# Optimization experiments

Measured on AMD Instinct MI355X. Metric: run time of the kernel, lower is better.

Reference implementation:

```python
import jax, jax.numpy as jnp
import numpy as np

K = 3  # sparsify_graph default k


def _lstm_dir(x, Wi, Wh, b, reverse):
    # x: [B, T, Hin]; Wi: [Hin, 4H]; Wh: [H, 4H]; b: [4H]
    B = x.shape[0]
    H = Wh.shape[0]
    xs = jnp.swapaxes(x, 0, 1)  # [T, B, Hin]
    if reverse:
        xs = xs[::-1]

    def step(carry, xt):
        h, c = carry
        g = xt @ Wi + h @ Wh + b
        i, f, gg, o = jnp.split(g, 4, axis=-1)  # torch gate order i,f,g,o
        c = jax.nn.sigmoid(f) * c + jax.nn.sigmoid(i) * jnp.tanh(gg)
        h = jax.nn.sigmoid(o) * jnp.tanh(c)
        return (h, c), h

    h0 = jnp.zeros((B, H), x.dtype)
    _, hs = jax.lax.scan(step, (h0, h0), xs)
    if reverse:
        hs = hs[::-1]
    return jnp.swapaxes(hs, 0, 1)  # [B, T, H]


def setup_inputs() -> dict:
    key = jax.random.key(0)
    ks = jax.random.split(key, 24)
    B, T, C, F = 16, 256, 64, 128
    GO, H = 32, 32  # gat_out, lstm hidden
    s = 0.1
    return {
        "x": jax.random.normal(ks[0], (B, T, C, F), jnp.float32),
        "spectral_w": jax.random.normal(ks[1], (C, F), jnp.float32),
        "gat_W": jax.random.normal(ks[2], (F, GO), jnp.float32) * s,
        "gat_a": jax.random.normal(ks[3], (2 * GO,), jnp.float32),
        "pool_w": jax.random.normal(ks[4], (GO, 1), jnp.float32) * s,
        "pool_b": jnp.zeros((1,), jnp.float32),
        "lstm_Wi_f": jax.random.normal(ks[5], (GO, 4 * H), jnp.float32) * s,
        "lstm_Wh_f": jax.random.normal(ks[6], (H, 4 * H), jnp.float32) * s,
        "lstm_b_f": jnp.zeros((4 * H,), jnp.float32),
        "lstm_Wi_r": jax.random.normal(ks[7], (GO, 4 * H), jnp.float32) * s,
        "lstm_Wh_r": jax.random.normal(ks[8], (H, 4 * H), jnp.float32) * s,
        "lstm_b_r": jnp.zeros((4 * H,), jnp.float32),
        "ta_W": jax.random.normal(ks[9], (2 * H, 2 * H), jnp.float32) * s,
        "ta_b": jnp.zeros((2 * H,), jnp.float32),
        "ta_v": jax.random.normal(ks[10], (2 * H,), jnp.float32) * s,
        "ln_g": jnp.ones((2 * H,), jnp.float32),
        "ln_b": jnp.zeros((2 * H,), jnp.float32),
        "fc1_w": jax.random.normal(ks[11], (2 * H, 32), jnp.float32) * s,
        "fc1_b": jnp.zeros((32,), jnp.float32),
        "fc2_w": jax.random.normal(ks[12], (32, 3), jnp.float32) * s,
        "fc2_b": jnp.zeros((3,), jnp.float32),
    }


def reference(x, spectral_w, gat_W, gat_a, pool_w, pool_b,
              lstm_Wi_f, lstm_Wh_f, lstm_b_f, lstm_Wi_r, lstm_Wh_r, lstm_b_r,
              ta_W, ta_b, ta_v, ln_g, ln_b, fc1_w, fc1_b, fc2_w, fc2_b):
    B, T, C, F = x.shape
    # SpectralWeighting: per-(channel,feature) softmaxed weights over feature dim
    x = x * jax.nn.softmax(spectral_w, axis=-1)  # [B,T,C,F]

    # compute_graph per sample: mean_t of cosine-similarity Gram over channels
    Hn = x / (jnp.linalg.norm(x, axis=-1, keepdims=True) + 1e-8)
    A = jnp.einsum('btcf,btdf->bcd', Hn, Hn) / T  # [B,C,C]

    # sparsify_graph: per-row top-(K+1), drop diagonal, symmetrize mask
    _, idx = jax.lax.top_k(A, K + 1)  # [B,C,K+1]
    topk_mask = jnp.sum(jax.nn.one_hot(idx, C, dtype=jnp.float32), axis=2) > 0  # [B,C,C]
    eye = jnp.eye(C, dtype=bool)
    topk_mask = topk_mask & ~eye
    topk_mask = topk_mask | jnp.swapaxes(topk_mask, 1, 2)
    A = jnp.where(topk_mask, A, 0.0)

    # GAT layer, vectorized over (B, T) with shared per-sample adjacency
    Wh = jnp.einsum('btcf,fo->btco', x, gat_W)  # [B,T,C,32]
    O = Wh.shape[-1]
    s1 = Wh @ gat_a[:O]  # [B,T,C]  a . Wh_i
    s2 = Wh @ gat_a[O:]  # [B,T,C]  a . Wh_j
    e = jax.nn.leaky_relu(s1[..., :, None] + s2[..., None, :], 0.2)  # [B,T,C,C]
    amask = (A > 0) | eye  # [B,C,C]
    e = jnp.where(amask[:, None], e, -1e9)
    alpha = jax.nn.softmax(e, axis=-1)  # dropout skipped (eval mode)
    gat = jax.nn.relu(jnp.einsum('btcd,btdo->btco', alpha, Wh))  # [B,T,C,32]

    # ChannelAttentionPooling: softmax over channel dim
    w = jax.nn.softmax(gat @ pool_w + pool_b, axis=2)  # [B,T,C,1]
    h = jnp.sum(gat * w, axis=2)  # [B,T,32]

    # BiLSTM
    hf = _lstm_dir(h, lstm_Wi_f, lstm_Wh_f, lstm_b_f, False)
    hr = _lstm_dir(h, lstm_Wi_r, lstm_Wh_r, lstm_b_r, True)
    h = jnp.concatenate([hf, hr], axis=-1)  # [B,T,64]

    # TemporalAttention (dropout skipped, eval mode)
    sc = (jnp.tanh(h @ ta_W + ta_b) @ ta_v) / 1.5  # [B,T]
    al = jax.nn.softmax(sc, axis=1)
    ctx = jnp.sum(h * al[..., None], axis=1)  # [B,64]

    # LayerNorm
    mu = jnp.mean(ctx, axis=-1, keepdims=True)
    var = jnp.var(ctx, axis=-1, keepdims=True)
    ctx = (ctx - mu) / jnp.sqrt(var + 1e-5) * ln_g + ln_b

    # Classifier head (dropout skipped, eval mode)
    return jax.nn.relu(ctx @ fc1_w + fc1_b) @ fc2_w + fc2_b  # [B,3]
```

## Files before the change

### kernel.cpp

```cpp
#include <hip/hip_runtime.h>
#include <hip/hip_bf16.h>

#define B_  16
#define T_  256
#define C_  64
#define F_  128
#define O_  32
#define H_  32
#define G4_ 128

typedef __attribute__((ext_vector_type(8))) short bfrag;
typedef __attribute__((ext_vector_type(4))) float f4acc;
typedef __attribute__((ext_vector_type(2))) float f2;

__device__ __forceinline__ unsigned short f2bf(float v) {
    union { float f; unsigned u; } c; c.f = v;
    unsigned r = c.u + 0x7FFF + ((c.u >> 16) & 1);
    return (unsigned short)(r >> 16);
}
__device__ __forceinline__ float bf2f(unsigned short b) {
    union { float f; unsigned u; } c; c.u = ((unsigned)b) << 16; return c.f;
}
__device__ __forceinline__ float sigm_f(float x) {
    return __builtin_amdgcn_rcpf(1.f + __expf(-x));
}
__device__ __forceinline__ float tanh_f(float x) {
    float e = __expf(2.f * x);
    return 1.f - 2.f * __builtin_amdgcn_rcpf(e + 1.f);
}
__device__ __forceinline__ float readlane_f(float v, int l) {
    return __int_as_float(__builtin_amdgcn_readlane(__float_as_int(v), l));
}

__global__ __launch_bounds__(64) void k_sw(const float* __restrict__ w,
                                           float* __restrict__ sw) {
    int c = blockIdx.x, lane = threadIdx.x;
    const float* row = w + c * F_;
    float v0 = row[lane], v1 = row[lane + 64];
    float m = fmaxf(v0, v1);
#pragma unroll
    for (int s = 1; s < 64; s <<= 1) m = fmaxf(m, __shfl_xor(m, s));
    float e0 = __expf(v0 - m), e1 = __expf(v1 - m);
    float s = e0 + e1;
#pragma unroll
    for (int s_ = 1; s_ < 64; s_ <<= 1) s += __shfl_xor(s, s_);
    sw[c * F_ + lane] = e0 / s;
    sw[c * F_ + lane + 64] = e1 / s;
}

#define TCP 4
#define PSTR 136

#define MFMA16(a, b, c) __builtin_amdgcn_mfma_f32_16x16x32_bf16(a, b, c, 0, 0, 0)

__global__ __launch_bounds__(256) void k_phase1(
    const float* __restrict__ x, const float* __restrict__ sw,
    const float* __restrict__ gat_W, const float* __restrict__ gat_a,
    float* __restrict__ A, float* __restrict__ Wh,
    float* __restrict__ s1, float* __restrict__ s2) {
    const int b = blockIdx.x, tc = blockIdx.y, tid = threadIdx.x;
    const int wv = tid >> 6, lane = tid & 63;
    const int quad = lane >> 4, l16 = lane & 15;

    __shared__ unsigned short hhi[64 * PSTR];
    __shared__ unsigned short hlo[64 * PSTR];
    __shared__ float nrm[64];
    __shared__ float s1p[2][64], s2p[2][64];

    float4 swr[8];
    {
        const float4* sw4 = (const float4*)sw;
#pragma unroll
        for (int i = 0; i < 8; i++) swr[i] = sw4[tid + 256 * i];
    }

    const int rt0 = (wv >> 1) * 2;
    const int ct0 = (wv & 1) * 2;
    const int jW = wv & 1;

    bfrag wfh[4], wfl[4];
    {
        const int n = l16 + 16 * jW;
#pragma unroll
        for (int k = 0; k < 4; k++) {
            union { unsigned short u[8]; bfrag v; } Hu, Lu;
#pragma unroll
            for (int u = 0; u < 8; u++) {
                float v = gat_W[(32 * k + quad * 8 + u) * O_ + n];
                unsigned short hb = f2bf(v);
                Hu.u[u] = hb;
                Lu.u[u] = f2bf(v - bf2f(hb));
            }
            wfh[k] = Hu.v;
            wfl[k] = Lu.v;
        }
    }
    const float ga1 = gat_a[l16 + 16 * jW];
    const float ga2 = gat_a[O_ + l16 + 16 * jW];

    f4acc accA[2][2];
#pragma unroll
    for (int i = 0; i < 2; i++)
#pragma unroll
        for (int j = 0; j < 2; j++) accA[i][j] = (f4acc){0.f, 0.f, 0.f, 0.f};

    for (int tt = 0; tt < TCP; ++tt) {
        const int t = tc * TCP + tt;
        const float4* xg = (const float4*)(x + ((size_t)(b * T_ + t) << 13));
        float4 xr[8];
#pragma unroll
        for (int i = 0; i < 8; i++) xr[i] = xg[tid + 256 * i];

        __syncthreads();

        float invn_[8];
#pragma unroll
        for (int i = 0; i < 8; i++) {
            float4 v = xr[i], s = swr[i];
            v.x *= s.x; v.y *= s.y; v.z *= s.z; v.w *= s.w;
            xr[i] = v;
            float ss = v.x * v.x + v.y * v.y + v.z * v.z + v.w * v.w;
#pragma unroll
            for (int d = 1; d < 32; d <<= 1) ss += __shfl_xor(ss, d);
            float nv = sqrtf(ss) + 1e-8f;
            invn_[i] = 1.0f / nv;
            if ((tid & 31) == 0) nrm[(tid >> 5) + 8 * i] = nv;
        }
#pragma unroll
        for (int i = 0; i < 8; i++) {
            int c = (tid >> 5) + 8 * i;
            float4 v = xr[i];
            float iv = invn_[i];
            float a0 = v.x * iv, a1 = v.y * iv, a2 = v.z * iv, a3 = v.w * iv;
            union { unsigned short u[4]; unsigned long long q; } Hq, Lq;
            unsigned short h0 = f2bf(a0), h1 = f2bf(a1), h2 = f2bf(a2), h3 = f2bf(a3);
            Hq.u[0] = h0; Hq.u[1] = h1; Hq.u[2] = h2; Hq.u[3] = h3;
            Lq.u[0] = f2bf(a0 - bf2f(h0));
            Lq.u[1] = f2bf(a1 - bf2f(h1));
            Lq.u[2] = f2bf(a2 - bf2f(h2));
            Lq.u[3] = f2bf(a3 - bf2f(h3));
            int off = c * PSTR + 4 * (tid & 31);
            *(unsigned long long*)&hhi[off] = Hq.q;
            *(unsigned long long*)&hlo[off] = Lq.q;
        }
        __syncthreads();

        f4acc accW0 = (f4acc){0.f, 0.f, 0.f, 0.f};
        f4acc accW1 = (f4acc){0.f, 0.f, 0.f, 0.f};
#pragma unroll
        for (int k = 0; k < 4; k++) {
            const int ko = 32 * k + 8 * quad;
            bfrag r0h = *(const bfrag*)&hhi[(rt0 * 16 + l16) * PSTR + ko];
            bfrag r0l = *(const bfrag*)&hlo[(rt0 * 16 + l16) * PSTR + ko];
            bfrag r1h = *(const bfrag*)&hhi[((rt0 + 1) * 16 + l16) * PSTR + ko];
            bfrag r1l = *(const bfrag*)&hlo[((rt0 + 1) * 16 + l16) * PSTR + ko];
            bfrag c0h = *(const bfrag*)&hhi[(ct0 * 16 + l16) * PSTR + ko];
            bfrag c0l = *(const bfrag*)&hlo[(ct0 * 16 + l16) * PSTR + ko];
            bfrag c1h = *(const bfrag*)&hhi[((ct0 + 1) * 16 + l16) * PSTR + ko];
            bfrag c1l = *(const bfrag*)&hlo[((ct0 + 1) * 16 + l16) * PSTR + ko];
            accA[0][0] = MFMA16(r0h, c0h, accA[0][0]);
            accA[0][0] = MFMA16(r0h, c0l, accA[0][0]);
            accA[0][0] = MFMA16(r0l, c0h, accA[0][0]);
            accA[0][1] = MFMA16(r0h, c1h, accA[0][1]);
            accA[0][1] = MFMA16(r0h, c1l, accA[0][1]);
            accA[0][1] = MFMA16(r0l, c1h, accA[0][1]);
            accA[1][0] = MFMA16(r1h, c0h, accA[1][0]);
            accA[1][0] = MFMA16(r1h, c0l, accA[1][0]);
            accA[1][0] = MFMA16(r1l, c0h, accA[1][0]);
            accA[1][1] = MFMA16(r1h, c1h, accA[1][1]);
            accA[1][1] = MFMA16(r1h, c1l, accA[1][1]);
            accA[1][1] = MFMA16(r1l, c1h, accA[1][1]);
            accW0 = MFMA16(r0h, wfh[k], accW0);
            accW0 = MFMA16(r0h, wfl[k], accW0);
            accW0 = MFMA16(r0l, wfh[k], accW0);
            accW1 = MFMA16(r1h, wfh[k], accW1);
            accW1 = MFMA16(r1h, wfl[k], accW1);
            accW1 = MFMA16(r1l, wfh[k], accW1);
        }
        float* whout = Wh + (size_t)(b * T_ + t) * (C_ * O_);
#pragma unroll
        for (int i2 = 0; i2 < 2; i2++) {
            f4acc aw = i2 ? accW1 : accW0;
#pragma unroll
            for (int r = 0; r < 4; r++) {
                int row = (rt0 + i2) * 16 + quad * 4 + r;
                float val = aw[r] * nrm[row];
                whout[row * O_ + l16 + 16 * jW] = val;
                float v1 = val * ga1, v2 = val * ga2;
#pragma unroll
                for (int d = 1; d < 16; d <<= 1) {
                    v1 += __shfl_xor(v1, d);
                    v2 += __shfl_xor(v2, d);
                }
                if (l16 == 0) { s1p[jW][row] = v1; s2p[jW][row] = v2; }
            }
        }
        __syncthreads();
        if (tid < 64) {
            s1[(b * T_ + t) * C_ + tid] = s1p[0][tid] + s1p[1][tid];
            s2[(b * T_ + t) * C_ + tid] = s2p[0][tid] + s2p[1][tid];
        }
    }
#pragma unroll
    for (int i2 = 0; i2 < 2; i2++)
#pragma unroll
        for (int j2 = 0; j2 < 2; j2++)
#pragma unroll
            for (int r = 0; r < 4; r++) {
                int row = (rt0 + i2) * 16 + quad * 4 + r;
                int col = (ct0 + j2) * 16 + l16;
                atomicAdd(&A[b * (C_ * C_) + row * C_ + col], accA[i2][j2][r]);
            }
}

__global__ __launch_bounds__(64) void k_topk(const float* __restrict__ A,
                                             unsigned long long* __restrict__ amask) {
    int b = blockIdx.x;
    int c = threadIdx.x;
    __shared__ unsigned long long tk[C_];
    const float* row = A + b * (C_ * C_) + c * C_;
    unsigned long long sel = 0ULL;
    for (int r = 0; r < 4; r++) {
        float best = -1e30f;
        int bi = 0;
        for (int d = 0; d < C_; d++) {
            if (sel & (1ULL << d)) continue;
            float v = row[d];
            if (v > best) { best = v; bi = d; }
        }
        sel |= (1ULL << bi);
    }
    unsigned long long t = sel & ~(1ULL << c);
    tk[c] = t;
    __syncthreads();
    unsigned long long sym = t;
    for (int d = 0; d < C_; d++)
        if ((tk[d] >> c) & 1ULL) sym |= (1ULL << d);
    unsigned long long m = (1ULL << c);
    unsigned long long s2 = sym;
    while (s2) {
        int d = __ffsll(s2) - 1;
        s2 &= s2 - 1;
        if (row[d] > 0.f) m |= (1ULL << d);
    }
    amask[b * C_ + c] = m;
}

__global__ __launch_bounds__(256) void k_gat(
    const float* __restrict__ Wh, const float* __restrict__ s1,
    const float* __restrict__ s2, const unsigned long long* __restrict__ amask,
    const float* __restrict__ pool_w, const float* __restrict__ pool_b,
    float* __restrict__ hout) {
    int tg = blockIdx.x;
    int wv = threadIdx.x >> 6, c = threadIdx.x & 63;
    int bt = tg * 4 + wv;
    int b = bt >> 8;
    __shared__ float buf[4][C_][33];
    __shared__ float s2s[4][C_];

    s2s[wv][c] = s2[bt * C_ + c];
    float s1c = s1[bt * C_ + c];
    unsigned long long m = amask[b * C_ + c];
    __syncthreads();

    float mx = -1e30f;
    unsigned long long mm = m;
    while (mm) {
        int d = __ffsll(mm) - 1; mm &= mm - 1;
        float v = s1c + s2s[wv][d];
        v = v > 0.f ? v : 0.2f * v;
        mx = fmaxf(mx, v);
    }
    float ssum = 0.f;
    mm = m;
    while (mm) {
        int d = __ffsll(mm) - 1; mm &= mm - 1;
        float v = s1c + s2s[wv][d];
        v = v > 0.f ? v : 0.2f * v;
        ssum += __expf(v - mx);
    }
    float inv = 1.0f / ssum;
    float g[O_];
#pragma unroll
    for (int i = 0; i < O_; i++) g[i] = 0.f;
    mm = m;
    while (mm) {
        int d = __ffsll(mm) - 1; mm &= mm - 1;
        float v = s1c + s2s[wv][d];
        v = v > 0.f ? v : 0.2f * v;
        float a = __expf(v - mx);
        const float4* wr = (const float4*)(Wh + (size_t)bt * (C_ * O_) + d * O_);
#pragma unroll
        for (int q = 0; q < 8; q++) {
            float4 w4 = wr[q];
            g[4 * q + 0] += a * w4.x;
            g[4 * q + 1] += a * w4.y;
            g[4 * q + 2] += a * w4.z;
            g[4 * q + 3] += a * w4.w;
        }
    }
    float lg = pool_b[0];
#pragma unroll
    for (int i = 0; i < O_; i++) {
        g[i] = fmaxf(g[i] * inv, 0.f);
        lg += g[i] * pool_w[i];
    }
    float wmx = lg;
#pragma unroll
    for (int s = 1; s < 64; s <<= 1) wmx = fmaxf(wmx, __shfl_xor(wmx, s));
    float we = __expf(lg - wmx);
    float wsum = we;
#pragma unroll
    for (int s = 1; s < 64; s <<= 1) wsum += __shfl_xor(wsum, s);
    float wcf = we / wsum;
#pragma unroll
    for (int i = 0; i < O_; i++) buf[wv][c][i] = g[i] * wcf;
    __syncthreads();
    {
        int wt = threadIdx.x >> 6, o = threadIdx.x & 31, hf = (threadIdx.x >> 5) & 1;
        float sacc = 0.f;
#pragma unroll 8
        for (int d = hf * 32; d < hf * 32 + 32; d++) sacc += buf[wt][d][o];
        sacc += __shfl_xor(sacc, 32);
        if (hf == 0) hout[(tg * 4 + wt) * O_ + o] = sacc;
    }
}

__global__ __launch_bounds__(128) void k_lstm_pre(
    const float* __restrict__ hin,
    const float* __restrict__ Wi_f, const float* __restrict__ b_f,
    const float* __restrict__ Wi_r, const float* __restrict__ b_r,
    float* __restrict__ gx) {
    int id = blockIdx.x;
    int dir = id >> 12;
    int bt = id & 4095;
    const float* Wi = dir ? Wi_r : Wi_f;
    const float* bb = dir ? b_r : b_f;
    int g = threadIdx.x;
    __shared__ float hs[H_];
    if (g < H_) hs[g] = hin[bt * O_ + g];
    __syncthreads();
    float acc = bb[g];
#pragma unroll
    for (int k = 0; k < H_; k++) acc += hs[k] * Wi[k * G4_ + g];
    gx[((size_t)dir * 4096 + bt) * G4_ + g] = acc;
}

#define WW(k) f2 ww##k = (f2){Wd[(k) * G4_ + lane], Wd[(k) * G4_ + lane + 64]};
#define KST2(k, Aq) { float hk = readlane_f(h, k); Aq += (f2){hk, hk} * ww##k; }
#define LDG(j, ss) { int sl = (ss); sl = sl < T_ ? sl : T_ - 1; \
    int tl = dir ? (T_ - 1 - sl) : sl; \
    p##j = (f2){gxb[tl * G4_ + lane], gxb[tl * G4_ + lane + 64]}; }
#define STEP(j, sbase) { \
    f2 A0 = p##j, A1 = (f2){0.f, 0.f}, A2 = (f2){0.f, 0.f}, A3 = (f2){0.f, 0.f}; \
    KST2(0, A0)  KST2(1, A1)  KST2(2, A2)  KST2(3, A3) \
    KST2(4, A0)  KST2(5, A1)  KST2(6, A2)  KST2(7, A3) \
    KST2(8, A0)  KST2(9, A1)  KST2(10, A2) KST2(11, A3) \
    KST2(12, A0) KST2(13, A1) KST2(14, A2) KST2(15, A3) \
    KST2(16, A0) KST2(17, A1) KST2(18, A2) KST2(19, A3) \
    KST2(20, A0) KST2(21, A1) KST2(22, A2) KST2(23, A3) \
    KST2(24, A0) KST2(25, A1) KST2(26, A2) KST2(27, A3) \
    KST2(28, A0) KST2(29, A1) KST2(30, A2) KST2(31, A3) \
    LDG(j, sbase + 8 + j) \
    f2 As = (A0 + A1) + (A2 + A3); \
    float sA = sigm_f(As.x); \
    float u = sigm_f(half_sel * As.y); \
    float sB = (lane < 32) ? fmaf(2.f, u, -1.f) : u; \
    float sf = __shfl_xor(sA, 32); \
    float so = __shfl_xor(sB, 32); \
    cst = fmaf(sf, cst, sA * sB); \
    float hn = so * tanh_f(cst); \
    h = hn; \
    if (lane < H_) hcat[((size_t)(b * T_) + tcur) * (2 * H_) + dir * H_ + lane] = hn; \
    tcur += dt; \
}

__global__ void __attribute__((amdgpu_flat_work_group_size(64, 64)))
__attribute__((amdgpu_waves_per_eu(1, 1))) k_lstm_seq(
    const float* __restrict__ gx,
    const float* __restrict__ Whf, const float* __restrict__ Whr,
    float* __restrict__ hcat) {
    int dir = blockIdx.x & 1, b = blockIdx.x >> 1;
    int lane = threadIdx.x;
    const float* Wd = dir ? Whr : Whf;
    WW(0) WW(1) WW(2) WW(3) WW(4) WW(5) WW(6) WW(7)
    WW(8) WW(9) WW(10) WW(11) WW(12) WW(13) WW(14) WW(15)
    WW(16) WW(17) WW(18) WW(19) WW(20) WW(21) WW(22) WW(23)
    WW(24) WW(25) WW(26) WW(27) WW(28) WW(29) WW(30) WW(31)

    const float* gxb = gx + ((size_t)dir * 4096 + b * T_) * G4_;
    float h = 0.f, cst = 0.f;
    const int dt = dir ? -1 : 1;
    int tcur = dir ? (T_ - 1) : 0;
    const float half_sel = (lane < 32) ? 2.f : 1.f;
    f2 p0, p1, p2, p3, p4, p5, p6, p7;
    LDG(0, 0) LDG(1, 1) LDG(2, 2) LDG(3, 3)
    LDG(4, 4) LDG(5, 5) LDG(6, 6) LDG(7, 7)
    for (int sb = 0; sb < T_; sb += 8) {
        STEP(0, sb) STEP(1, sb) STEP(2, sb) STEP(3, sb)
        STEP(4, sb) STEP(5, sb) STEP(6, sb) STEP(7, sb)
    }
}

__global__ __launch_bounds__(256) void k_final(
    const float* __restrict__ hcat,
    const float* __restrict__ taW, const float* __restrict__ tab,
    const float* __restrict__ tav,
    const float* __restrict__ lng, const float* __restrict__ lnb,
    const float* __restrict__ w1, const float* __restrict__ b1,
    const float* __restrict__ w2, const float* __restrict__ b2,
    float* __restrict__ out) {
    int b = blockIdx.x;
    int t = threadIdx.x;
    __shared__ float Wl[64 * 64];
    __shared__ float al[T_];
    __shared__ float wred[4];
    __shared__ float ctxp[4][64];
    __shared__ float ctx[64];
    __shared__ float a1[32];
    for (int i = t; i < 4096; i += 256) Wl[i] = taW[i];
    float4 hr[16];
    const float4* hb = (const float4*)(hcat + ((size_t)b * T_ + t) * 64);
#pragma unroll
    for (int i = 0; i < 16; i++) hr[i] = hb[i];
    __syncthreads();
    float sc = 0.f;
    for (int j = 0; j < 64; j++) {
        float s = tab[j];
#pragma unroll
        for (int k4 = 0; k4 < 16; k4++) {
            float4 h4 = hr[k4];
            const float* wcol = &Wl[(4 * k4) * 64 + j];
            s += h4.x * wcol[0] + h4.y * wcol[64] + h4.z * wcol[128] + h4.w * wcol[192];
        }
        sc += tanhf(s) * tav[j];
    }
    sc *= (1.0f / 1.5f);
    int wave = t >> 6, lane = t & 63;
    float m = sc;
#pragma unroll
    for (int s_ = 1; s_ < 64; s_ <<= 1) m = fmaxf(m, __shfl_xor(m, s_));
    if (lane == 0) wred[wave] = m;
    __syncthreads();
    m = fmaxf(fmaxf(wred[0], wred[1]), fmaxf(wred[2], wred[3]));
    float e = __expf(sc - m);
    float ssum = e;
#pragma unroll
    for (int s_ = 1; s_ < 64; s_ <<= 1) ssum += __shfl_xor(ssum, s_);
    __syncthreads();
    if (lane == 0) wred[wave] = ssum;
    __syncthreads();
    float S = wred[0] + wred[1] + wred[2] + wred[3];
    al[t] = e / S;
    __syncthreads();
    {
        int o = t & 63, part = t >> 6;
        float cacc = 0.f;
        for (int tt = part * 64; tt < part * 64 + 64; tt++)
            cacc += al[tt] * hcat[((size_t)b * T_ + tt) * 64 + o];
        ctxp[part][o] = cacc;
    }
    __syncthreads();
    if (t < 64) {
        float ctxo = ctxp[0][t] + ctxp[1][t] + ctxp[2][t] + ctxp[3][t];
        float sv = ctxo, sq = ctxo * ctxo;
#pragma unroll
        for (int s_ = 1; s_ < 64; s_ <<= 1) {
            sv += __shfl_xor(sv, s_);
            sq += __shfl_xor(sq, s_);
        }
        float mu = sv * (1.f / 64.f);
        float var = sq * (1.f / 64.f) - mu * mu;
        ctx[t] = (ctxo - mu) / sqrtf(var + 1e-5f) * lng[t] + lnb[t];
    }
    __syncthreads();
    if (t < 32) {
        float s = b1[t];
        for (int k = 0; k < 64; k++) s += ctx[k] * w1[k * 32 + t];
        a1[t] = fmaxf(s, 0.f);
    }
    __syncthreads();
    if (t < 3) {
        float s = b2[t];
        for (int k = 0; k < 32; k++) s += a1[k] * w2[k * 3 + t];
        out[b * 3 + t] = s;
    }
}

extern "C" void kernel_launch(void* const* d_in, const int* in_sizes, int n_in,
                              void* d_out, int out_size, void* d_ws, size_t ws_size,
                              hipStream_t stream) {
    const float* x          = (const float*)d_in[0];
    const float* spectral_w = (const float*)d_in[1];
    const float* gat_W      = (const float*)d_in[2];
    const float* gat_a      = (const float*)d_in[3];
    const float* pool_w     = (const float*)d_in[4];
    const float* pool_b     = (const float*)d_in[5];
    const float* lstm_Wi_f  = (const float*)d_in[6];
    const float* lstm_Wh_f  = (const float*)d_in[7];
    const float* lstm_b_f   = (const float*)d_in[8];
    const float* lstm_Wi_r  = (const float*)d_in[9];
    const float* lstm_Wh_r  = (const float*)d_in[10];
    const float* lstm_b_r   = (const float*)d_in[11];
    const float* ta_W       = (const float*)d_in[12];
    const float* ta_b       = (const float*)d_in[13];
    const float* ta_v       = (const float*)d_in[14];
    const float* ln_g       = (const float*)d_in[15];
    const float* ln_b       = (const float*)d_in[16];
    const float* fc1_w      = (const float*)d_in[17];
    const float* fc1_b      = (const float*)d_in[18];
    const float* fc2_w      = (const float*)d_in[19];
    const float* fc2_b      = (const float*)d_in[20];
    float* out = (float*)d_out;

    float* ws = (float*)d_ws;
    float* sw    = ws + 0;
    float* A     = ws + 8192;
    unsigned long long* amask = (unsigned long long*)(ws + 73728);
    float* Wh    = ws + 75776;
    float* s1    = ws + 8464384;
    float* s2    = ws + 8726528;
    float* hpool = ws + 8988672;
    float* gx    = ws + 9119744;
    float* hcat  = ws + 10168320;

    hipMemsetAsync(A, 0, (size_t)C_ * C_ * B_ * sizeof(float), stream);
    k_sw<<<C_, 64, 0, stream>>>(spectral_w, sw);
    k_phase1<<<dim3(B_, T_ / TCP), 256, 0, stream>>>(x, sw, gat_W, gat_a, A, Wh, s1, s2);
    k_topk<<<B_, 64, 0, stream>>>(A, amask);
    k_gat<<<B_ * T_ / 4, 256, 0, stream>>>(Wh, s1, s2, amask, pool_w, pool_b, hpool);
    k_lstm_pre<<<2 * B_ * T_, 128, 0, stream>>>(hpool, lstm_Wi_f, lstm_b_f,
                                                lstm_Wi_r, lstm_b_r, gx);
    k_lstm_seq<<<2 * B_, 64, 0, stream>>>(gx, lstm_Wh_f, lstm_Wh_r, hcat);
    k_final<<<B_, 256, 0, stream>>>(hcat, ta_W, ta_b, ta_v, ln_g, ln_b,
                                    fc1_w, fc1_b, fc2_w, fc2_b, out);
}
```

Before: 442.2 us.

## Interleave LSTM gate layout so each lane computes all four gates

The input-projection kernel now stores the gate pre-activations interleaved per hidden unit (i,f,g,o next to each other). The recurrent kernel changes so each lane holds all four gate weights for one hidden unit as a float4 and computes every gate locally. This removes the two cross-half-wave shuffles on the serial recurrence path. In exchange each lane does twice the FMAs, the upper 32 lanes duplicate the work, the two accumulator chains are deeper, and the gx prefetch depth drops from 8 to 4 steps.

```diff
diff --git a/kernel.cpp b/kernel.cpp
--- a/kernel.cpp
+++ b/kernel.cpp
@@ -12,6 +12,7 @@
 typedef __attribute__((ext_vector_type(8))) short bfrag;
 typedef __attribute__((ext_vector_type(4))) float f4acc;
 typedef __attribute__((ext_vector_type(2))) float f2;
+typedef __attribute__((ext_vector_type(4))) float f4;
 
 __device__ __forceinline__ unsigned short f2bf(float v) {
     union { float f; unsigned u; } c; c.f = v;
@@ -343,35 +344,35 @@
     float acc = bb[g];
 #pragma unroll
     for (int k = 0; k < H_; k++) acc += hs[k] * Wi[k * G4_ + g];
-    gx[((size_t)dir * 4096 + bt) * G4_ + g] = acc;
-}
-
-#define WW(k) f2 ww##k = (f2){Wd[(k) * G4_ + lane], Wd[(k) * G4_ + lane + 64]};
-#define KST2(k, Aq) { float hk = readlane_f(h, k); Aq += (f2){hk, hk} * ww##k; }
-#define LDG(j, ss) { int sl = (ss); sl = sl < T_ ? sl : T_ - 1; \
+    int j = g & 31, gate = g >> 5;
+    gx[((size_t)dir * 4096 + bt) * G4_ + j * 4 + gate] = acc;
+}
+
+#define WW(k) f4 ww##k = (f4){Wd[(k) * G4_ + j], Wd[(k) * G4_ + j + 32], \
+                              Wd[(k) * G4_ + j + 64], Wd[(k) * G4_ + j + 96]};
+#define KST(k, Aq) { float hk = readlane_f(h, k); Aq += ww##k * hk; }
+#define LDG(slot, ss) { int sl = (ss); sl = sl < T_ ? sl : T_ - 1; \
     int tl = dir ? (T_ - 1 - sl) : sl; \
-    p##j = (f2){gxb[tl * G4_ + lane], gxb[tl * G4_ + lane + 64]}; }
-#define STEP(j, sbase) { \
-    f2 A0 = p##j, A1 = (f2){0.f, 0.f}, A2 = (f2){0.f, 0.f}, A3 = (f2){0.f, 0.f}; \
-    KST2(0, A0)  KST2(1, A1)  KST2(2, A2)  KST2(3, A3) \
-    KST2(4, A0)  KST2(5, A1)  KST2(6, A2)  KST2(7, A3) \
-    KST2(8, A0)  KST2(9, A1)  KST2(10, A2) KST2(11, A3) \
-    KST2(12, A0) KST2(13, A1) KST2(14, A2) KST2(15, A3) \
-    KST2(16, A0) KST2(17, A1) KST2(18, A2) KST2(19, A3) \
-    KST2(20, A0) KST2(21, A1) KST2(22, A2) KST2(23, A3) \
-    KST2(24, A0) KST2(25, A1) KST2(26, A2) KST2(27, A3) \
-    KST2(28, A0) KST2(29, A1) KST2(30, A2) KST2(31, A3) \
-    LDG(j, sbase + 8 + j) \
-    f2 As = (A0 + A1) + (A2 + A3); \
-    float sA = sigm_f(As.x); \
-    float u = sigm_f(half_sel * As.y); \
-    float sB = (lane < 32) ? fmaf(2.f, u, -1.f) : u; \
-    float sf = __shfl_xor(sA, 32); \
-    float so = __shfl_xor(sB, 32); \
-    cst = fmaf(sf, cst, sA * sB); \
-    float hn = so * tanh_f(cst); \
-    h = hn; \
-    if (lane < H_) hcat[((size_t)(b * T_) + tcur) * (2 * H_) + dir * H_ + lane] = hn; \
+    p##slot = *(const f4*)(gxb + tl * G4_ + 4 * j); }
+#define STEP(slot, sbase) { \
+    f4 A0 = p##slot, A1 = (f4){0.f, 0.f, 0.f, 0.f}; \
+    KST(0, A0)  KST(1, A1)  KST(2, A0)  KST(3, A1) \
+    KST(4, A0)  KST(5, A1)  KST(6, A0)  KST(7, A1) \
+    KST(8, A0)  KST(9, A1)  KST(10, A0) KST(11, A1) \
+    KST(12, A0) KST(13, A1) KST(14, A0) KST(15, A1) \
+    KST(16, A0) KST(17, A1) KST(18, A0) KST(19, A1) \
+    KST(20, A0) KST(21, A1) KST(22, A0) KST(23, A1) \
+    KST(24, A0) KST(25, A1) KST(26, A0) KST(27, A1) \
+    KST(28, A0) KST(29, A1) KST(30, A0) KST(31, A1) \
+    LDG(slot, sbase + 4 + slot) \
+    f4 G = A0 + A1; \
+    float si = sigm_f(G.x); \
+    float sf = sigm_f(G.y); \
+    float tg = tanh_f(G.z); \
+    float so = sigm_f(G.w); \
+    cst = fmaf(sf, cst, si * tg); \
+    h = so * tanh_f(cst); \
+    if (lane < H_) hcat[((size_t)(b * T_) + tcur) * (2 * H_) + dir * H_ + j] = h; \
     tcur += dt; \
 }
 
@@ -382,6 +383,7 @@
     float* __restrict__ hcat) {
     int dir = blockIdx.x & 1, b = blockIdx.x >> 1;
     int lane = threadIdx.x;
+    int j = lane & 31;
     const float* Wd = dir ? Whr : Whf;
     WW(0) WW(1) WW(2) WW(3) WW(4) WW(5) WW(6) WW(7)
     WW(8) WW(9) WW(10) WW(11) WW(12) WW(13) WW(14) WW(15)
@@ -392,13 +394,10 @@
     float h = 0.f, cst = 0.f;
     const int dt = dir ? -1 : 1;
     int tcur = dir ? (T_ - 1) : 0;
-    const float half_sel = (lane < 32) ? 2.f : 1.f;
-    f2 p0, p1, p2, p3, p4, p5, p6, p7;
+    f4 p0, p1, p2, p3;
     LDG(0, 0) LDG(1, 1) LDG(2, 2) LDG(3, 3)
-    LDG(4, 4) LDG(5, 5) LDG(6, 6) LDG(7, 7)
-    for (int sb = 0; sb < T_; sb += 8) {
+    for (int sb = 0; sb < T_; sb += 4) {
         STEP(0, sb) STEP(1, sb) STEP(2, sb) STEP(3, sb)
-        STEP(4, sb) STEP(5, sb) STEP(6, sb) STEP(7, sb)
     }
 }
 
```

New measurement: 452.1 us. +2.2%, slower.
